# Kernel tuning notes

Hardware: AMD Instinct MI355X
Metric: run time of the kernel (lower is better)

Reference implementation:

```python
import jax, jax.numpy as jnp
import numpy as np

N, E, H = 50000, 800000, 4
IN, HID, OUT = 128, 64, 16
SIM_THRESH = 0.1
NEG_SLOPE = 0.01  # F.leaky_relu default


def setup_inputs() -> dict:
    key = jax.random.key(0)
    k = jax.random.split(key, 6)
    x = jax.random.normal(k[0], (N, IN), jnp.float32)
    row = jax.random.randint(k[1], (E,), 0, N)
    col = jax.random.randint(k[2], (E,), 0, N)
    W0 = jax.random.normal(k[3], (H, IN, HID), jnp.float32) / np.float32(np.sqrt(IN))
    W1 = jax.random.normal(k[4], (H, H * HID, HID), jnp.float32) / np.float32(np.sqrt(H * HID))
    W2 = jax.random.normal(k[5], (1, H * HID, OUT), jnp.float32) / np.float32(np.sqrt(H * HID))
    return {"x": x, "W0": W0, "W1": W1, "W2": W2, "row": row, "col": col}


def _att_coef(x, row, col):
    # cosine similarity on edges only (honors the sparse edge structure)
    nrm = jnp.linalg.norm(x, axis=1, keepdims=True)
    xn = x / jnp.maximum(nrm, 1e-12)
    sim = jnp.sum(xn[row] * xn[col], axis=1)            # [E]
    sim = jnp.where(sim < SIM_THRESH, 0.0, sim)
    # L1 row-normalize the thresholded attention matrix
    rowsum = jax.ops.segment_sum(jnp.abs(sim), row, num_segments=N)
    rs_e = rowsum[row]
    att = jnp.where(rs_e > 0, sim / jnp.where(rs_e > 0, rs_e, 1.0), 0.0)
    # degree-based self-loop weight lam = 1/(deg+1), then exp of all nonzeros
    deg = jax.ops.segment_sum((att != 0).astype(x.dtype), row, num_segments=N)
    w_edge = jnp.where(att != 0, jnp.exp(att), 0.0)     # zero entries stay zero (dropped nnz)
    w_self = jnp.exp(1.0 / (deg + 1.0))                 # [N]
    return w_edge, w_self


def _layer(x, W, row, col, act):
    w_edge, w_self = _att_coef(x, row, col)
    z = jnp.einsum('nd,hdo->nho', x, W)                 # per-head projection
    msg = w_edge[:, None, None] * z[col]                # [E,h,o] gather + weight
    agg = jax.ops.segment_sum(msg, row, num_segments=N) + w_self[:, None, None] * z
    out = agg.reshape(N, -1)                            # concat heads (flatten(1))
    return jax.nn.leaky_relu(out, NEG_SLOPE) if act else out


def reference(x, W0, W1, W2, row, col):
    h = _layer(x, W0, row, col, True)
    h = _layer(h, W1, row, col, True)
    h = _layer(h, W2, row, col, False)
    return h
```

## Files before the change

### kernel.cpp

```cpp
#include <hip/hip_runtime.h>
#include <math.h>


static inline int cdiv(int a, int b){ return (a + b - 1) / b; }


__device__ inline float vdot(float4 a, float4 b){ return a.x*b.x + a.y*b.y + a.z*b.z + a.w*b.w; }
__device__ inline void vfma(float4& acc, float w, float4 b){
  acc.x += w*b.x; acc.y += w*b.y; acc.z += w*b.z; acc.w += w*b.w;
}
__device__ inline float4 vscale(float w, float4 a){ return make_float4(w*a.x, w*a.y, w*a.z, w*a.w); }

__device__ inline float wred(float d){
  #pragma unroll
  for (int off = 32; off; off >>= 1) d += __shfl_xor(d, off);
  return d;
}

__device__ inline unsigned short f2bf(float f){
  unsigned int u = __float_as_uint(f);
  unsigned int r = (u + 0x7FFFu + ((u >> 16) & 1u)) >> 16;
  return (unsigned short)r;
}
__device__ inline float bf2f(unsigned int us){ return __uint_as_float(us << 16); }

__device__ inline void bf8_to_f(uint4 v, float* f){
  f[0] = bf2f(v.x & 0xFFFFu); f[1] = bf2f(v.x >> 16);
  f[2] = bf2f(v.y & 0xFFFFu); f[3] = bf2f(v.y >> 16);
  f[4] = bf2f(v.z & 0xFFFFu); f[5] = bf2f(v.z >> 16);
  f[6] = bf2f(v.w & 0xFFFFu); f[7] = bf2f(v.w >> 16);
}


__global__ void count_kernel(const int* __restrict__ row, int* __restrict__ cnt, int E){
  int e = blockIdx.x * blockDim.x + threadIdx.x;
  if (e < E) atomicAdd(&cnt[row[e]], 1);
}

__global__ void scan1_kernel(const int* __restrict__ cnt, int* __restrict__ offs,
                             int* __restrict__ bsum, int n){
  __shared__ int tmp[256];
  int tid = threadIdx.x;
  int g = blockIdx.x * 256 + tid;
  int v = (g < n) ? cnt[g] : 0;
  tmp[tid] = v;
  __syncthreads();
  for (int off = 1; off < 256; off <<= 1){
    int t = (tid >= off) ? tmp[tid - off] : 0;
    __syncthreads();
    tmp[tid] += t;
    __syncthreads();
  }
  if (g < n) offs[g] = tmp[tid] - v;
  if (tid == 255) bsum[blockIdx.x] = tmp[255];
}

__global__ void scan2_kernel(int* __restrict__ bsum, int* __restrict__ offs, int nb, int n){
  __shared__ int tmp[256];
  int tid = threadIdx.x;
  int v = (tid < nb) ? bsum[tid] : 0;
  tmp[tid] = v;
  __syncthreads();
  for (int off = 1; off < 256; off <<= 1){
    int t = (tid >= off) ? tmp[tid - off] : 0;
    __syncthreads();
    tmp[tid] += t;
    __syncthreads();
  }
  if (tid < nb) bsum[tid] = tmp[tid] - v;
  if (tid == 255) offs[n] = tmp[255];
}

__global__ void scan3_kernel(int* __restrict__ offs, int* __restrict__ cur,
                             const int* __restrict__ bsum, int n){
  int g = blockIdx.x * 256 + threadIdx.x;
  if (g < n){
    int o = offs[g] + bsum[blockIdx.x];
    offs[g] = o;
    cur[g]  = o;
  }
}

__global__ void scatter_kernel(const int* __restrict__ row, const int* __restrict__ col,
                               int* __restrict__ cur, int* __restrict__ ecol, int E){
  int e = blockIdx.x * blockDim.x + threadIdx.x;
  if (e < E){
    int p = atomicAdd(&cur[row[e]], 1);
    ecol[p] = col[e];
  }
}


__global__ void invnorm128_kernel(const float* __restrict__ x, float* __restrict__ invn, int N){
  int n = blockIdx.x * 4 + (threadIdx.x >> 6);
  int lane = threadIdx.x & 63;
  if (n >= N) return;
  float2 a = ((const float2*)(x + (size_t)n * 128))[lane];
  float ss = a.x * a.x + a.y * a.y;
  ss = wred(ss);
  if (lane == 0) invn[n] = 1.0f / fmaxf(sqrtf(ss), 1e-12f);
}


template<int R>
__global__ void att_agg_wave128(const float* __restrict__ x, const float* __restrict__ invn,
                                const int* __restrict__ offs, const int* __restrict__ ecol,
                                float* __restrict__ out, int N){
  constexpr int LT = 64;
  __shared__ float tls[4][LT];
  __shared__ int   tlk[4][LT];
  const int wid  = threadIdx.x >> 6;
  const int lane = threadIdx.x & 63;
  const int half = lane >> 5, hl = lane & 31;
  const int hidx = wid * 2 + half;
  const int n = blockIdx.x * 2 + wid;
  if (n >= N) return;
  const int s = offs[n], e = offs[n + 1];
  const float inr = invn[n];
  const float4* xv = (const float4*)x;
  float4 a = xv[(size_t)n * 32 + hl];

  float4 br[R];
  float  simv[R];
  float  rowsum = 0.0f;
  int    deg = 0;

  #pragma unroll
  for (int r = 0; r < R; r++){
    simv[r] = 0.0f;
    int k = s + 2 * r + half;
    if (k < e){
      int c = ecol[k];
      float4 b = xv[(size_t)c * 32 + hl];
      br[r] = b;
      float d = vdot(a, b);
      #pragma unroll
      for (int off = 16; off; off >>= 1) d += __shfl_xor(d, off);
      d *= inr * invn[c];
      if (d < 0.1f) d = 0.0f;
      simv[r] = d;
      rowsum += d;
      deg += (d != 0.0f) ? 1 : 0;
    }
  }

  int tc = 0, kover = e;
  int k = s + 2 * R + half;
  for (; k + 2 < e; k += 4){
    int c0 = ecol[k], c1 = ecol[k + 2];
    float4 b0 = xv[(size_t)c0 * 32 + hl];
    float4 b1 = xv[(size_t)c1 * 32 + hl];
    float d0 = vdot(a, b0), d1 = vdot(a, b1);
    #pragma unroll
    for (int off = 16; off; off >>= 1){ d0 += __shfl_xor(d0, off); d1 += __shfl_xor(d1, off); }
    d0 *= inr * invn[c0];
    d1 *= inr * invn[c1];
    if (d0 < 0.1f) d0 = 0.0f;
    if (d1 < 0.1f) d1 = 0.0f;
    rowsum += d0 + d1;
    deg += (d0 != 0.0f) + (d1 != 0.0f);
    if (d0 > 0.0f){
      if (tc < LT){ if (hl == 0){ tls[hidx][tc] = d0; tlk[hidx][tc] = c0; } tc++; }
      else if (kover > k) kover = k;
    }
    if (d1 > 0.0f){
      if (tc < LT){ if (hl == 0){ tls[hidx][tc] = d1; tlk[hidx][tc] = c1; } tc++; }
      else if (kover > k + 2) kover = k + 2;
    }
  }
  if (k < e){
    int c0 = ecol[k];
    float4 b0 = xv[(size_t)c0 * 32 + hl];
    float d0 = vdot(a, b0);
    #pragma unroll
    for (int off = 16; off; off >>= 1) d0 += __shfl_xor(d0, off);
    d0 *= inr * invn[c0];
    if (d0 < 0.1f) d0 = 0.0f;
    rowsum += d0;
    deg += (d0 != 0.0f) ? 1 : 0;
    if (d0 > 0.0f){
      if (tc < LT){ if (hl == 0){ tls[hidx][tc] = d0; tlk[hidx][tc] = c0; } tc++; }
      else if (kover > k) kover = k;
    }
  }

  rowsum += __shfl_xor(rowsum, 32);
  deg    += __shfl_xor(deg, 32);
  const float invrs = (rowsum > 0.0f) ? 1.0f / rowsum : 0.0f;
  const float wself = expf(1.0f / (float)(deg + 1));

  float4 acc = (half == 0) ? vscale(wself, a) : make_float4(0.f, 0.f, 0.f, 0.f);
  #pragma unroll
  for (int r = 0; r < R; r++){
    if (simv[r] > 0.0f) vfma(acc, expf(simv[r] * invrs), br[r]);
  }
  int j = 0;
  for (; j + 1 < tc; j += 2){
    float w0 = expf(tls[hidx][j] * invrs);
    float w1 = expf(tls[hidx][j + 1] * invrs);
    int c0 = tlk[hidx][j], c1 = tlk[hidx][j + 1];
    float4 b0 = xv[(size_t)c0 * 32 + hl];
    float4 b1 = xv[(size_t)c1 * 32 + hl];
    vfma(acc, w0, b0);
    vfma(acc, w1, b1);
  }
  if (j < tc){
    float w0 = expf(tls[hidx][j] * invrs);
    float4 b0 = xv[(size_t)tlk[hidx][j] * 32 + hl];
    vfma(acc, w0, b0);
  }
  for (int k2 = kover; k2 < e; k2 += 2){
    int c = ecol[k2];
    float4 b = xv[(size_t)c * 32 + hl];
    float d = vdot(a, b);
    #pragma unroll
    for (int off = 16; off; off >>= 1) d += __shfl_xor(d, off);
    d *= inr * invn[c];
    if (d >= 0.1f) vfma(acc, expf(d * invrs), b);
  }

  acc.x += __shfl_xor(acc.x, 32);
  acc.y += __shfl_xor(acc.y, 32);
  acc.z += __shfl_xor(acc.z, 32);
  acc.w += __shfl_xor(acc.w, 32);
  if (half == 0) ((float4*)out)[(size_t)n * 32 + hl] = acc;
}


template<int R>
__global__ void att_agg_wave256(const float* __restrict__ x, const float* __restrict__ invn,
                                const int* __restrict__ offs, const int* __restrict__ ecol,
                                float* __restrict__ out, int N){
  constexpr int LT = 64;
  __shared__ float tls[2][LT];
  __shared__ int   tlk[2][LT];
  const int wid  = threadIdx.x >> 6;
  const int lane = threadIdx.x & 63;
  const int n = blockIdx.x * 2 + wid;
  if (n >= N) return;
  const int s = offs[n], e = offs[n + 1];
  const float inr = invn[n];
  const float4* xv = (const float4*)x;
  float4 a = xv[(size_t)n * 64 + lane];

  float4 br[R];
  float  simv[R];
  float  rowsum = 0.0f;
  int    deg = 0;

  #pragma unroll
  for (int r = 0; r < R; r++){
    simv[r] = 0.0f;
    if (s + r < e){
      int c = ecol[s + r];
      float4 b = xv[(size_t)c * 64 + lane];
      br[r] = b;
      float d = wred(vdot(a, b)) * inr * invn[c];
      if (d < 0.1f) d = 0.0f;
      simv[r] = d;
      rowsum += d;
      deg += (d != 0.0f) ? 1 : 0;
    }
  }

  int tc = 0, kover = e;
  int k = s + R;
  for (; k + 1 < e; k += 2){
    int c0 = ecol[k], c1 = ecol[k + 1];
    float4 b0 = xv[(size_t)c0 * 64 + lane];
    float4 b1 = xv[(size_t)c1 * 64 + lane];
    float d0 = wred(vdot(a, b0)) * inr * invn[c0];
    float d1 = wred(vdot(a, b1)) * inr * invn[c1];
    if (d0 < 0.1f) d0 = 0.0f;
    if (d1 < 0.1f) d1 = 0.0f;
    rowsum += d0 + d1;
    deg += (d0 != 0.0f) + (d1 != 0.0f);
    if (d0 > 0.0f){
      if (tc < LT){ if (lane == 0){ tls[wid][tc] = d0; tlk[wid][tc] = c0; } tc++; }
      else if (kover > k) kover = k;
    }
    if (d1 > 0.0f){
      if (tc < LT){ if (lane == 0){ tls[wid][tc] = d1; tlk[wid][tc] = c1; } tc++; }
      else if (kover > k + 1) kover = k + 1;
    }
  }
  if (k < e){
    int c0 = ecol[k];
    float4 b0 = xv[(size_t)c0 * 64 + lane];
    float d0 = wred(vdot(a, b0)) * inr * invn[c0];
    if (d0 < 0.1f) d0 = 0.0f;
    rowsum += d0;
    deg += (d0 != 0.0f) ? 1 : 0;
    if (d0 > 0.0f){
      if (tc < LT){ if (lane == 0){ tls[wid][tc] = d0; tlk[wid][tc] = c0; } tc++; }
      else if (kover > k) kover = k;
    }
  }

  const float invrs = (rowsum > 0.0f) ? 1.0f / rowsum : 0.0f;
  const float wself = expf(1.0f / (float)(deg + 1));

  float4 acc = vscale(wself, a);
  #pragma unroll
  for (int r = 0; r < R; r++){
    if (simv[r] > 0.0f) vfma(acc, expf(simv[r] * invrs), br[r]);
  }
  int j = 0;
  for (; j + 1 < tc; j += 2){
    float w0 = expf(tls[wid][j] * invrs);
    float w1 = expf(tls[wid][j + 1] * invrs);
    int c0 = tlk[wid][j], c1 = tlk[wid][j + 1];
    float4 b0 = xv[(size_t)c0 * 64 + lane];
    float4 b1 = xv[(size_t)c1 * 64 + lane];
    vfma(acc, w0, b0);
    vfma(acc, w1, b1);
  }
  if (j < tc){
    float w0 = expf(tls[wid][j] * invrs);
    float4 b0 = xv[(size_t)tlk[wid][j] * 64 + lane];
    vfma(acc, w0, b0);
  }
  for (int k2 = kover; k2 < e; k2++){
    int c = ecol[k2];
    float4 b = xv[(size_t)c * 64 + lane];
    float d = wred(vdot(a, b)) * inr * invn[c];
    if (d >= 0.1f) vfma(acc, expf(d * invrs), b);
  }

  ((float4*)out)[(size_t)n * 64 + lane] = acc;
}


__global__ void att_z16_bf(const unsigned short* __restrict__ hbf,
                           const float* __restrict__ invn,
                           const int* __restrict__ offs, const int* __restrict__ ecol,
                           const float* __restrict__ z2, float* __restrict__ out, int N){
  constexpr int LT = 64;
  __shared__ float tls[4][LT];
  __shared__ int   tlk[4][LT];
  const int wid  = threadIdx.x >> 6;
  const int lane = threadIdx.x & 63;
  const int half = lane >> 5, hl = lane & 31;
  const int hidx = wid * 2 + half;
  const int n = blockIdx.x * 2 + wid;
  if (n >= N) return;
  const int s = offs[n], e = offs[n + 1];
  const float inr = invn[n];
  const uint4* hb = (const uint4*)hbf;

  float a8[8];
  bf8_to_f(hb[(size_t)n * 32 + hl], a8);

  float rowsum = 0.0f;
  int   deg = 0;
  int   tc = 0, kover = e;

  int k = s + half;
  for (; k + 2 < e; k += 4){
    int c0 = ecol[k], c1 = ecol[k + 2];
    uint4 v0 = hb[(size_t)c0 * 32 + hl];
    uint4 v1 = hb[(size_t)c1 * 32 + hl];
    float b0[8], b1[8];
    bf8_to_f(v0, b0);
    bf8_to_f(v1, b1);
    float d0 = 0.0f, d1 = 0.0f;
    #pragma unroll
    for (int t = 0; t < 8; t++){ d0 += a8[t] * b0[t]; d1 += a8[t] * b1[t]; }
    #pragma unroll
    for (int off = 16; off; off >>= 1){ d0 += __shfl_xor(d0, off); d1 += __shfl_xor(d1, off); }
    d0 *= inr * invn[c0];
    d1 *= inr * invn[c1];
    if (d0 < 0.1f) d0 = 0.0f;
    if (d1 < 0.1f) d1 = 0.0f;
    rowsum += d0 + d1;
    deg += (d0 != 0.0f) + (d1 != 0.0f);
    if (d0 > 0.0f){
      if (tc < LT){ if (hl == 0){ tls[hidx][tc] = d0; tlk[hidx][tc] = c0; } tc++; }
      else if (kover > k) kover = k;
    }
    if (d1 > 0.0f){
      if (tc < LT){ if (hl == 0){ tls[hidx][tc] = d1; tlk[hidx][tc] = c1; } tc++; }
      else if (kover > k + 2) kover = k + 2;
    }
  }
  if (k < e){
    int c0 = ecol[k];
    uint4 v0 = hb[(size_t)c0 * 32 + hl];
    float b0[8];
    bf8_to_f(v0, b0);
    float d0 = 0.0f;
    #pragma unroll
    for (int t = 0; t < 8; t++) d0 += a8[t] * b0[t];
    #pragma unroll
    for (int off = 16; off; off >>= 1) d0 += __shfl_xor(d0, off);
    d0 *= inr * invn[c0];
    if (d0 < 0.1f) d0 = 0.0f;
    rowsum += d0;
    deg += (d0 != 0.0f) ? 1 : 0;
    if (d0 > 0.0f){
      if (tc < LT){ if (hl == 0){ tls[hidx][tc] = d0; tlk[hidx][tc] = c0; } tc++; }
      else if (kover > k) kover = k;
    }
  }

  rowsum += __shfl_xor(rowsum, 32);
  deg    += __shfl_xor(deg, 32);
  const float invrs = (rowsum > 0.0f) ? 1.0f / rowsum : 0.0f;
  const float wself = expf(1.0f / (float)(deg + 1));

  const int grp = hl >> 4, ch = hl & 15;
  float acc = 0.0f;
  for (int j = grp; j < tc; j += 2){
    float w = expf(tls[hidx][j] * invrs);
    int   c = tlk[hidx][j];
    acc += w * z2[(size_t)c * 16 + ch];
  }
  for (int k2 = kover; k2 < e; k2 += 4){
    int c = ecol[k2];
    uint4 v = hb[(size_t)c * 32 + hl];
    float b[8];
    bf8_to_f(v, b);
    float d = 0.0f;
    #pragma unroll
    for (int t = 0; t < 8; t++) d += a8[t] * b[t];
    #pragma unroll
    for (int off = 16; off; off >>= 1) d += __shfl_xor(d, off);
    d *= inr * invn[c];
    if (d >= 0.1f){
      float w = expf(d * invrs);
      if (grp == 0) acc += w * z2[(size_t)c * 16 + ch];
    }
  }
  acc += __shfl_xor(acc, 16);
  acc += __shfl_xor(acc, 32);
  if (lane < 16) out[(size_t)n * 16 + lane] = acc + wself * z2[(size_t)n * 16 + lane];
}


template<int D>
__global__ void proj_act_norm(const float* __restrict__ xin, const float* __restrict__ W,
                              float* __restrict__ hout, float* __restrict__ invn,
                              unsigned short* __restrict__ hbf, int N){
  __shared__ float xs[16][D];
  __shared__ float red[4][16];
  int tid = threadIdx.x;
  int n0 = blockIdx.x * 16;
  for (int i = tid; i < 16 * D; i += 256){
    int nl = i / D, d = i % D;
    int n = n0 + nl;
    xs[nl][d] = (n < N) ? xin[(size_t)n * D + d] : 0.0f;
  }
  __syncthreads();
  int h = tid >> 6, o = tid & 63;
  const float* Wp = W + (size_t)h * D * 64 + o;
  float acc[16];
  #pragma unroll
  for (int i = 0; i < 16; i++) acc[i] = 0.0f;
  for (int d = 0; d < D; d++){
    float w = Wp[(size_t)d * 64];
    #pragma unroll
    for (int i = 0; i < 16; i++) acc[i] += xs[i][d] * w;
  }
  #pragma unroll
  for (int i = 0; i < 16; i++){
    float a = acc[i];
    acc[i] = (a > 0.0f) ? a : 0.01f * a;
  }
  #pragma unroll
  for (int i = 0; i < 16; i++){
    int n = n0 + i;
    if (n < N){
      hout[(size_t)n * 256 + tid] = acc[i];
      if (hbf) hbf[(size_t)n * 256 + tid] = f2bf(acc[i]);
    }
  }
  int wave = tid >> 6, lane = tid & 63;
  #pragma unroll
  for (int i = 0; i < 16; i++){
    float ss = acc[i] * acc[i];
    ss = wred(ss);
    if (lane == 0) red[wave][i] = ss;
  }
  __syncthreads();
  if (tid < 16){
    int n = n0 + tid;
    if (n < N){
      float t = red[0][tid] + red[1][tid] + red[2][tid] + red[3][tid];
      invn[n] = 1.0f / fmaxf(sqrtf(t), 1e-12f);
    }
  }
}

__global__ void proj16_kernel(const float* __restrict__ x, const float* __restrict__ W,
                              float* __restrict__ z, int N){
  __shared__ float xs[16][256];
  __shared__ float wsh[256 * 16];
  int tid = threadIdx.x;
  int n0 = blockIdx.x * 16;
  for (int i = tid; i < 16 * 256; i += 256){
    int nl = i >> 8, d = i & 255;
    int n = n0 + nl;
    xs[nl][d] = (n < N) ? x[(size_t)n * 256 + d] : 0.0f;
  }
  for (int i = tid; i < 256 * 16; i += 256) wsh[i] = W[i];
  __syncthreads();
  int nl = tid >> 4, o = tid & 15;
  float acc = 0.0f;
  for (int d = 0; d < 256; d++) acc += xs[nl][d] * wsh[d * 16 + o];
  int n = n0 + nl;
  if (n < N) z[(size_t)n * 16 + o] = acc;
}


extern "C" void kernel_launch(void* const* d_in, const int* in_sizes, int n_in,
                              void* d_out, int out_size, void* d_ws, size_t ws_size,
                              hipStream_t stream){
  const float* x  = (const float*)d_in[0];
  const float* W0 = (const float*)d_in[1];
  const float* W1 = (const float*)d_in[2];
  const float* W2 = (const float*)d_in[3];
  const int*   row = (const int*)d_in[4];
  const int*   col = (const int*)d_in[5];
  const int N = in_sizes[0] / 128;
  const int E = in_sizes[4];
  float* out = (float*)d_out;

  float* p = (float*)d_ws;
  float* hbuf   = p; p += (size_t)N * 256;
  float* aggbuf = p; p += (size_t)N * 256;
  float* z2     = p; p += (size_t)N * 16;
  float* invn   = p; p += N;
  unsigned short* hbf = (unsigned short*)p; p += (size_t)N * 128;
  int* cnt  = (int*)p;
  int* offs = cnt + N;
  int* cur  = offs + N + 1;
  int* ecol = cur + N;
  int* bsum = ecol + E;

  const int NB = cdiv(N, 256);

  hipMemsetAsync(cnt, 0, sizeof(int) * N, stream);
  count_kernel<<<cdiv(E, 256), 256, 0, stream>>>(row, cnt, E);
  scan1_kernel<<<NB, 256, 0, stream>>>(cnt, offs, bsum, N);
  scan2_kernel<<<1, 256, 0, stream>>>(bsum, offs, NB, N);
  scan3_kernel<<<NB, 256, 0, stream>>>(offs, cur, bsum, N);
  scatter_kernel<<<cdiv(E, 256), 256, 0, stream>>>(row, col, cur, ecol, E);

  invnorm128_kernel<<<cdiv(N, 4), 256, 0, stream>>>(x, invn, N);
  att_agg_wave128<8><<<cdiv(N, 2), 128, 0, stream>>>(x, invn, offs, ecol, aggbuf, N);
  proj_act_norm<128><<<cdiv(N, 16), 256, 0, stream>>>(aggbuf, W0, hbuf, invn, nullptr, N);

  att_agg_wave256<8><<<cdiv(N, 2), 128, 0, stream>>>(hbuf, invn, offs, ecol, aggbuf, N);
  proj_act_norm<256><<<cdiv(N, 16), 256, 0, stream>>>(aggbuf, W1, hbuf, invn, hbf, N);

  proj16_kernel<<<cdiv(N, 16), 256, 0, stream>>>(hbuf, W2, z2, N);
  att_z16_bf<<<cdiv(N, 2), 128, 0, stream>>>(hbf, invn, offs, ecol, z2, out, N);
}
```

Baseline: 794.2 us.

## Use bf16 features and half-wave edge splitting in layer-2 attention aggregation

The second-layer attention/aggregation kernel now reads a bf16 copy of the hidden features, which the first projection now also writes, instead of fp32. Each wave splits into two 32-lane halves that handle alternate edges, with rowsum, degree and accumulators combined across halves at the end. This halves the bytes gathered per neighbor row and doubles edge-level parallelism per wave, at the cost of bf16 rounding in both the similarity and the aggregated values. The overflow-path stride in the final kernel is also changed from 4 to 2.

New measurement: 723.7 us. 1.1x faster.

```diff
diff --git a/kernel.cpp b/kernel.cpp
--- a/kernel.cpp
+++ b/kernel.cpp
@@ -228,34 +228,46 @@
 
 
 template<int R>
-__global__ void att_agg_wave256(const float* __restrict__ x, const float* __restrict__ invn,
-                                const int* __restrict__ offs, const int* __restrict__ ecol,
-                                float* __restrict__ out, int N){
+__global__ void att256_bf(const unsigned short* __restrict__ hbf,
+                          const float* __restrict__ invn,
+                          const int* __restrict__ offs, const int* __restrict__ ecol,
+                          float* __restrict__ out, int N){
   constexpr int LT = 64;
-  __shared__ float tls[2][LT];
-  __shared__ int   tlk[2][LT];
+  __shared__ float tls[4][LT];
+  __shared__ int   tlk[4][LT];
   const int wid  = threadIdx.x >> 6;
   const int lane = threadIdx.x & 63;
+  const int half = lane >> 5, hl = lane & 31;
+  const int hidx = wid * 2 + half;
   const int n = blockIdx.x * 2 + wid;
   if (n >= N) return;
   const int s = offs[n], e = offs[n + 1];
   const float inr = invn[n];
-  const float4* xv = (const float4*)x;
-  float4 a = xv[(size_t)n * 64 + lane];
-
-  float4 br[R];
-  float  simv[R];
-  float  rowsum = 0.0f;
-  int    deg = 0;
+  const uint4* hb = (const uint4*)hbf;
+
+  float a8[8];
+  bf8_to_f(hb[(size_t)n * 32 + hl], a8);
+
+  uint4 brv[R];
+  float simv[R];
+  float rowsum = 0.0f;
+  int   deg = 0;
 
   #pragma unroll
   for (int r = 0; r < R; r++){
     simv[r] = 0.0f;
-    if (s + r < e){
-      int c = ecol[s + r];
-      float4 b = xv[(size_t)c * 64 + lane];
-      br[r] = b;
-      float d = wred(vdot(a, b)) * inr * invn[c];
+    int k = s + 2 * r + half;
+    if (k < e){
+      int c = ecol[k];
+      uint4 v = hb[(size_t)c * 32 + hl];
+      brv[r] = v;
+      float b8[8]; bf8_to_f(v, b8);
+      float d = 0.0f;
+      #pragma unroll
+      for (int t = 0; t < 8; t++) d += a8[t] * b8[t];
+      #pragma unroll
+      for (int off = 16; off; off >>= 1) d += __shfl_xor(d, off);
+      d *= inr * invn[c];
       if (d < 0.1f) d = 0.0f;
       simv[r] = d;
       rowsum += d;
@@ -264,70 +276,113 @@
   }
 
   int tc = 0, kover = e;
-  int k = s + R;
-  for (; k + 1 < e; k += 2){
-    int c0 = ecol[k], c1 = ecol[k + 1];
-    float4 b0 = xv[(size_t)c0 * 64 + lane];
-    float4 b1 = xv[(size_t)c1 * 64 + lane];
-    float d0 = wred(vdot(a, b0)) * inr * invn[c0];
-    float d1 = wred(vdot(a, b1)) * inr * invn[c1];
+  int k = s + 2 * R + half;
+  for (; k + 2 < e; k += 4){
+    int c0 = ecol[k], c1 = ecol[k + 2];
+    uint4 v0 = hb[(size_t)c0 * 32 + hl];
+    uint4 v1 = hb[(size_t)c1 * 32 + hl];
+    float b0[8], b1[8];
+    bf8_to_f(v0, b0);
+    bf8_to_f(v1, b1);
+    float d0 = 0.0f, d1 = 0.0f;
+    #pragma unroll
+    for (int t = 0; t < 8; t++){ d0 += a8[t] * b0[t]; d1 += a8[t] * b1[t]; }
+    #pragma unroll
+    for (int off = 16; off; off >>= 1){ d0 += __shfl_xor(d0, off); d1 += __shfl_xor(d1, off); }
+    d0 *= inr * invn[c0];
+    d1 *= inr * invn[c1];
     if (d0 < 0.1f) d0 = 0.0f;
     if (d1 < 0.1f) d1 = 0.0f;
     rowsum += d0 + d1;
     deg += (d0 != 0.0f) + (d1 != 0.0f);
     if (d0 > 0.0f){
-      if (tc < LT){ if (lane == 0){ tls[wid][tc] = d0; tlk[wid][tc] = c0; } tc++; }
+      if (tc < LT){ if (hl == 0){ tls[hidx][tc] = d0; tlk[hidx][tc] = c0; } tc++; }
       else if (kover > k) kover = k;
     }
     if (d1 > 0.0f){
-      if (tc < LT){ if (lane == 0){ tls[wid][tc] = d1; tlk[wid][tc] = c1; } tc++; }
-      else if (kover > k + 1) kover = k + 1;
+      if (tc < LT){ if (hl == 0){ tls[hidx][tc] = d1; tlk[hidx][tc] = c1; } tc++; }
+      else if (kover > k + 2) kover = k + 2;
     }
   }
   if (k < e){
     int c0 = ecol[k];
-    float4 b0 = xv[(size_t)c0 * 64 + lane];
-    float d0 = wred(vdot(a, b0)) * inr * invn[c0];
+    uint4 v0 = hb[(size_t)c0 * 32 + hl];
+    float b0[8]; bf8_to_f(v0, b0);
+    float d0 = 0.0f;
+    #pragma unroll
+    for (int t = 0; t < 8; t++) d0 += a8[t] * b0[t];
+    #pragma unroll
+    for (int off = 16; off; off >>= 1) d0 += __shfl_xor(d0, off);
+    d0 *= inr * invn[c0];
     if (d0 < 0.1f) d0 = 0.0f;
     rowsum += d0;
     deg += (d0 != 0.0f) ? 1 : 0;
     if (d0 > 0.0f){
-      if (tc < LT){ if (lane == 0){ tls[wid][tc] = d0; tlk[wid][tc] = c0; } tc++; }
+      if (tc < LT){ if (hl == 0){ tls[hidx][tc] = d0; tlk[hidx][tc] = c0; } tc++; }
       else if (kover > k) kover = k;
     }
   }
 
+  rowsum += __shfl_xor(rowsum, 32);
+  deg    += __shfl_xor(deg, 32);
   const float invrs = (rowsum > 0.0f) ? 1.0f / rowsum : 0.0f;
   const float wself = expf(1.0f / (float)(deg + 1));
 
-  float4 acc = vscale(wself, a);
+  float acc8[8];
+  #pragma unroll
+  for (int t = 0; t < 8; t++) acc8[t] = (half == 0) ? wself * a8[t] : 0.0f;
   #pragma unroll
   for (int r = 0; r < R; r++){
-    if (simv[r] > 0.0f) vfma(acc, expf(simv[r] * invrs), br[r]);
+    if (simv[r] > 0.0f){
+      float w = expf(simv[r] * invrs);
+      float b8[8]; bf8_to_f(brv[r], b8);
+      #pragma unroll
+      for (int t = 0; t < 8; t++) acc8[t] += w * b8[t];
+    }
   }
   int j = 0;
   for (; j + 1 < tc; j += 2){
-    float w0 = expf(tls[wid][j] * invrs);
-    float w1 = expf(tls[wid][j + 1] * invrs);
-    int c0 = tlk[wid][j], c1 = tlk[wid][j + 1];
-    float4 b0 = xv[(size_t)c0 * 64 + lane];
-    float4 b1 = xv[(size_t)c1 * 64 + lane];
-    vfma(acc, w0, b0);
-    vfma(acc, w1, b1);
+    float w0 = expf(tls[hidx][j] * invrs);
+    float w1 = expf(tls[hidx][j + 1] * invrs);
+    uint4 v0 = hb[(size_t)tlk[hidx][j] * 32 + hl];
+    uint4 v1 = hb[(size_t)tlk[hidx][j + 1] * 32 + hl];
+    float b0[8], b1[8];
+    bf8_to_f(v0, b0);
+    bf8_to_f(v1, b1);
+    #pragma unroll
+    for (int t = 0; t < 8; t++) acc8[t] += w0 * b0[t] + w1 * b1[t];
   }
   if (j < tc){
-    float w0 = expf(tls[wid][j] * invrs);
-    float4 b0 = xv[(size_t)tlk[wid][j] * 64 + lane];
-    vfma(acc, w0, b0);
-  }
-  for (int k2 = kover; k2 < e; k2++){
+    float w0 = expf(tls[hidx][j] * invrs);
+    uint4 v0 = hb[(size_t)tlk[hidx][j] * 32 + hl];
+    float b0[8]; bf8_to_f(v0, b0);
+    #pragma unroll
+    for (int t = 0; t < 8; t++) acc8[t] += w0 * b0[t];
+  }
+  for (int k2 = kover; k2 < e; k2 += 2){
     int c = ecol[k2];
-    float4 b = xv[(size_t)c * 64 + lane];
-    float d = wred(vdot(a, b)) * inr * invn[c];
-    if (d >= 0.1f) vfma(acc, expf(d * invrs), b);
-  }
-
-  ((float4*)out)[(size_t)n * 64 + lane] = acc;
+    uint4 v = hb[(size_t)c * 32 + hl];
+    float b[8]; bf8_to_f(v, b);
+    float d = 0.0f;
+    #pragma unroll
+    for (int t = 0; t < 8; t++) d += a8[t] * b[t];
+    #pragma unroll
+    for (int off = 16; off; off >>= 1) d += __shfl_xor(d, off);
+    d *= inr * invn[c];
+    if (d >= 0.1f){
+      float w = expf(d * invrs);
+      #pragma unroll
+      for (int t = 0; t < 8; t++) acc8[t] += w * b[t];
+    }
+  }
+
+  #pragma unroll
+  for (int t = 0; t < 8; t++) acc8[t] += __shfl_xor(acc8[t], 32);
+  if (half == 0){
+    float4* ov = (float4*)out;
+    ov[(size_t)n * 64 + 2 * hl]     = make_float4(acc8[0], acc8[1], acc8[2], acc8[3]);
+    ov[(size_t)n * 64 + 2 * hl + 1] = make_float4(acc8[4], acc8[5], acc8[6], acc8[7]);
+  }
 }
 
 
@@ -386,8 +441,7 @@
   if (k < e){
     int c0 = ecol[k];
     uint4 v0 = hb[(size_t)c0 * 32 + hl];
-    float b0[8];
-    bf8_to_f(v0, b0);
+    float b0[8]; bf8_to_f(v0, b0);
     float d0 = 0.0f;
     #pragma unroll
     for (int t = 0; t < 8; t++) d0 += a8[t] * b0[t];
@@ -415,11 +469,10 @@
     int   c = tlk[hidx][j];
     acc += w * z2[(size_t)c * 16 + ch];
   }
-  for (int k2 = kover; k2 < e; k2 += 4){
+  for (int k2 = kover; k2 < e; k2 += 2){
     int c = ecol[k2];
     uint4 v = hb[(size_t)c * 32 + hl];
-    float b[8];
-    bf8_to_f(v, b);
+    float b[8]; bf8_to_f(v, b);
     float d = 0.0f;
     #pragma unroll
     for (int t = 0; t < 8; t++) d += a8[t] * b[t];
@@ -548,9 +601,9 @@
 
   invnorm128_kernel<<<cdiv(N, 4), 256, 0, stream>>>(x, invn, N);
   att_agg_wave128<8><<<cdiv(N, 2), 128, 0, stream>>>(x, invn, offs, ecol, aggbuf, N);
-  proj_act_norm<128><<<cdiv(N, 16), 256, 0, stream>>>(aggbuf, W0, hbuf, invn, nullptr, N);
-
-  att_agg_wave256<8><<<cdiv(N, 2), 128, 0, stream>>>(hbuf, invn, offs, ecol, aggbuf, N);
+  proj_act_norm<128><<<cdiv(N, 16), 256, 0, stream>>>(aggbuf, W0, hbuf, invn, hbf, N);
+
+  att256_bf<4><<<cdiv(N, 2), 128, 0, stream>>>(hbf, invn, offs, ecol, aggbuf, N);
   proj_act_norm<256><<<cdiv(N, 16), 256, 0, stream>>>(aggbuf, W1, hbuf, invn, hbf, N);
 
   proj16_kernel<<<cdiv(N, 16), 256, 0, stream>>>(hbuf, W2, z2, N);
```
